# Kernel tuning notes

Measured on AMD Instinct MI355X. Metric: run time of the kernel, lower is better.

Reference implementation:

```python
import jax, jax.numpy as jnp
import numpy as np

B, T, IN_DIM, H = 128, 512, 128, 512


def _lstm_layer(x, W_ih, W_hh, b_ih, b_hh):
    """Single-layer batch-first LSTM (PyTorch gate order i,f,g,o).
    x: [B, T, D]. Returns (outputs [B, T, H], h_T [B, H], c_T [B, H])."""
    Bsz = x.shape[0]
    Hdim = W_hh.shape[1]
    # Precompute the input contribution for all timesteps: [T, B, 4H]
    xg = jnp.einsum('btd,gd->tbg', x, W_ih) + (b_ih + b_hh)

    def step(carry, xg_t):
        h, c = carry
        gates = xg_t + h @ W_hh.T  # [B, 4H]
        i, f, g, o = jnp.split(gates, 4, axis=-1)
        i = jax.nn.sigmoid(i)
        f = jax.nn.sigmoid(f)
        g = jnp.tanh(g)
        o = jax.nn.sigmoid(o)
        c = f * c + i * g
        h = o * jnp.tanh(c)
        return (h, c), h

    h0 = jnp.zeros((Bsz, Hdim), dtype=x.dtype)
    c0 = jnp.zeros((Bsz, Hdim), dtype=x.dtype)
    (hT, cT), outs = jax.lax.scan(step, (h0, c0), xg)
    return jnp.transpose(outs, (1, 0, 2)), hT, cT


def setup_inputs() -> dict:
    key = jax.random.key(0)
    ks = jax.random.split(key, 9)
    s1 = 1.0 / np.sqrt(H)
    inp = {
        'x': jax.random.normal(ks[0], (B, T, IN_DIM), dtype=jnp.float32),
        'W_ih1': jax.random.uniform(ks[1], (4 * H, IN_DIM), jnp.float32, -s1, s1),
        'W_hh1': jax.random.uniform(ks[2], (4 * H, H), jnp.float32, -s1, s1),
        'b_ih1': jax.random.uniform(ks[3], (4 * H,), jnp.float32, -s1, s1),
        'b_hh1': jax.random.uniform(ks[4], (4 * H,), jnp.float32, -s1, s1),
        'W_ih2': jax.random.uniform(ks[5], (4 * H, H), jnp.float32, -s1, s1),
        'W_hh2': jax.random.uniform(ks[6], (4 * H, H), jnp.float32, -s1, s1),
        'b_ih2': jax.random.uniform(ks[7], (4 * H,), jnp.float32, -s1, s1),
        'b_hh2': jax.random.uniform(ks[8], (4 * H,), jnp.float32, -s1, s1),
    }
    return inp


def reference(x, W_ih1, W_hh1, b_ih1, b_hh1, W_ih2, W_hh2, b_ih2, b_hh2):
    out1, _, _ = _lstm_layer(x, W_ih1, W_hh1, b_ih1, b_hh1)
    _, hT, cT = _lstm_layer(out1, W_ih2, W_hh2, b_ih2, b_hh2)
    # Match torch nn.LSTM final-state shape: [num_layers*dirs=1, B, H]
    return hT[None, :, :], cT[None, :, :]
```

## Files before the change

kernel.cpp:

```cpp
#include <hip/hip_runtime.h>
#include <stdint.h>
#include <stddef.h>


typedef __attribute__((ext_vector_type(8))) short short8;
typedef __attribute__((ext_vector_type(4))) float f32x4;
typedef unsigned long long u64;

#define DEV static __device__ __forceinline__
#define SCOPE_AGENT __HIP_MEMORY_SCOPE_AGENT

constexpr int TSEQ = 512;
constexpr int DIN  = 128;
constexpr int HDIM = 512;
constexpr int NCL  = 8;
constexpr int BB   = 16;
constexpr int NJ   = 32;
constexpr int COLS = 16;

DEV unsigned short f2bf(float f) {
  unsigned u = __float_as_uint(f);
  u += 0x7fffu + ((u >> 16) & 1u);
  return (unsigned short)(u >> 16);
}
DEV short8 pack8(float4 a, float4 b) {
  short8 r;
  r[0] = (short)f2bf(a.x); r[1] = (short)f2bf(a.y);
  r[2] = (short)f2bf(a.z); r[3] = (short)f2bf(a.w);
  r[4] = (short)f2bf(b.x); r[5] = (short)f2bf(b.y);
  r[6] = (short)f2bf(b.z); r[7] = (short)f2bf(b.w);
  return r;
}
DEV short8 mk8(u64 lo, u64 hi) {
  union { u64 q[2]; short8 v; } u;
  u.q[0] = lo; u.q[1] = hi; return u.v;
}
DEV f32x4 mfma16(short8 a, short8 b, f32x4 c) {
  return __builtin_amdgcn_mfma_f32_16x16x32_bf16(a, b, c, 0, 0, 0);
}
DEV float sigf(float v) { return 1.f / (1.f + __expf(-v)); }
DEV float tanh_(float v) {
  v = fminf(20.f, fmaxf(-20.f, v));
  float e = __expf(2.f * v);
  return (e - 1.f) / (e + 1.f);
}

__global__ void zero_ws(unsigned* p, int n) {
  int i = blockIdx.x * 256 + threadIdx.x;
  if (i < n)
    __hip_atomic_store(p + i, 0u, __ATOMIC_RELAXED, SCOPE_AGENT);
}

#define SWZ(row, idx) ((idx) ^ (((row) & 15) << 3))

__global__ __launch_bounds__(256, 1) void lstm_persist(
    const float* __restrict__ x,
    const float* __restrict__ Wih1, const float* __restrict__ Whh1,
    const float* __restrict__ bih1, const float* __restrict__ bhh1,
    const float* __restrict__ Wih2, const float* __restrict__ Whh2,
    const float* __restrict__ bih2, const float* __restrict__ bhh2,
    float* __restrict__ out,
    unsigned short* __restrict__ buf1,
    unsigned short* __restrict__ buf2,
    unsigned* __restrict__ flags)
{
  __shared__ short xs [16 * DIN];
  __shared__ short h1s[16 * HDIM];
  __shared__ short o1s[16 * HDIM];
  __shared__ short h2s[16 * HDIM];
  __shared__ float red1[4 * 16 * 66];
  __shared__ float red2[4 * 16 * 66];
  __shared__ float bias1s[64], bias2s[64];

  const int tid  = threadIdx.x;
  const int lane = tid & 63;
  const int lm   = lane & 15;
  const int lq   = lane >> 4;
  const int kq   = tid >> 6;

  const int bid     = blockIdx.x;
  const int cluster = bid & 7;
  const int j       = bid >> 3;
  const int cb      = cluster * BB;
  unsigned* flagA = flags + cluster * 64;
  unsigned* flagB = flags + cluster * 64 + NJ;

  short8 wf1[4][5];
  short8 wf2[4][8];
  #pragma unroll
  for (int g = 0; g < 4; ++g) {
    const int gr = g * HDIM + j * COLS + lm;
    #pragma unroll
    for (int sl = 0; sl < 5; ++sl) {
      const int k0 = (kq * 5 + sl) * 32 + 8 * lq;
      const float* src = (k0 < DIN) ? (Wih1 + (size_t)gr * DIN + k0)
                                    : (Whh1 + (size_t)gr * HDIM + (k0 - DIN));
      wf1[g][sl] = pack8(*(const float4*)src, *(const float4*)(src + 4));
    }
    #pragma unroll
    for (int sl = 0; sl < 8; ++sl) {
      const int k0 = (kq * 8 + sl) * 32 + 8 * lq;
      const float* src = (k0 < HDIM) ? (Wih2 + (size_t)gr * HDIM + k0)
                                     : (Whh2 + (size_t)gr * HDIM + (k0 - HDIM));
      wf2[g][sl] = pack8(*(const float4*)src, *(const float4*)(src + 4));
    }
  }
  if (tid < 64) {
    const int g = tid >> 4, nn = tid & 15;
    const int gr = g * HDIM + j * COLS + nn;
    bias1s[tid] = bih1[gr] + bhh1[gr];
    bias2s[tid] = bih2[gr] + bhh2[gr];
  }

  const int pm = tid >> 4, pnn = tid & 15;
  float c1 = 0.f, c2 = 0.f;

  for (int it = 0; it <= TSEQ + 2; ++it) {
    const bool l1 = (it < TSEQ);
    const bool l2 = (it >= 3);
    const int  t2 = it - 3;

    float4 xa, xb;
    if (l1) {
      const int row = tid >> 4, kc = tid & 15;
      const float* xp = x + ((size_t)(cb + row) * TSEQ + it) * DIN + kc * 8;
      xa = *(const float4*)xp; xb = *(const float4*)(xp + 4);
    }
    u64 o1t[8];
    if (l2) {
      const unsigned short* o1r =
          buf1 + (size_t)(((t2 & 3) * NCL + cluster) * BB) * HDIM;
      #pragma unroll
      for (int ci = 0; ci < 4; ++ci) {
        const int g = ci * 256 + tid, row = g >> 6, kc = g & 63;
        const u64* s = (const u64*)(o1r + (size_t)row * HDIM + kc * 8);
        o1t[2 * ci]     = __hip_atomic_load(s,     __ATOMIC_RELAXED, SCOPE_AGENT);
        o1t[2 * ci + 1] = __hip_atomic_load(s + 1, __ATOMIC_RELAXED, SCOPE_AGENT);
      }
    }

    if (it > 0) {
      if (kq == 0) {
        const unsigned tgtA = (unsigned)(l1 ? it : TSEQ);
        const unsigned tgtB = (it >= 4) ? (unsigned)(it - 1) : 0u;
        const unsigned tgt  = (lane < NJ) ? tgtA : tgtB;
        const unsigned* fl  = flagA + lane;
        while (true) {
          unsigned v = __hip_atomic_load(fl, __ATOMIC_RELAXED, SCOPE_AGENT);
          if (__all((int)(v >= tgt))) break;
          __builtin_amdgcn_s_sleep(1);
        }
      }
      __syncthreads();
    }

    if (l1) {
      const int row = tid >> 4, kc = tid & 15;
      *(short8*)(&xs[SWZ(row, row * DIN + kc * 8)]) = pack8(xa, xb);
    }
    if (l2) {
      #pragma unroll
      for (int ci = 0; ci < 4; ++ci) {
        const int g = ci * 256 + tid, row = g >> 6, kc = g & 63;
        *(short8*)(&o1s[SWZ(row, row * HDIM + kc * 8)]) =
            mk8(o1t[2 * ci], o1t[2 * ci + 1]);
      }
    }
    {
      u64 h1t[8], h2t[8];
      const unsigned short* h1r =
          buf1 + (size_t)((((it + 3) & 3) * NCL + cluster) * BB) * HDIM;
      const unsigned short* h2r =
          buf2 + (size_t)(((it & 1) * NCL + cluster) * BB) * HDIM;
      if (l1) {
        #pragma unroll
        for (int ci = 0; ci < 4; ++ci) {
          const int g = ci * 256 + tid, row = g >> 6, kc = g & 63;
          const u64* s = (const u64*)(h1r + (size_t)row * HDIM + kc * 8);
          h1t[2 * ci]     = __hip_atomic_load(s,     __ATOMIC_RELAXED, SCOPE_AGENT);
          h1t[2 * ci + 1] = __hip_atomic_load(s + 1, __ATOMIC_RELAXED, SCOPE_AGENT);
        }
      }
      if (l2) {
        #pragma unroll
        for (int ci = 0; ci < 4; ++ci) {
          const int g = ci * 256 + tid, row = g >> 6, kc = g & 63;
          const u64* s = (const u64*)(h2r + (size_t)row * HDIM + kc * 8);
          h2t[2 * ci]     = __hip_atomic_load(s,     __ATOMIC_RELAXED, SCOPE_AGENT);
          h2t[2 * ci + 1] = __hip_atomic_load(s + 1, __ATOMIC_RELAXED, SCOPE_AGENT);
        }
      }
      if (l1) {
        #pragma unroll
        for (int ci = 0; ci < 4; ++ci) {
          const int g = ci * 256 + tid, row = g >> 6, kc = g & 63;
          *(short8*)(&h1s[SWZ(row, row * HDIM + kc * 8)]) =
              mk8(h1t[2 * ci], h1t[2 * ci + 1]);
        }
      }
      if (l2) {
        #pragma unroll
        for (int ci = 0; ci < 4; ++ci) {
          const int g = ci * 256 + tid, row = g >> 6, kc = g & 63;
          *(short8*)(&h2s[SWZ(row, row * HDIM + kc * 8)]) =
              mk8(h2t[2 * ci], h2t[2 * ci + 1]);
        }
      }
    }
    __syncthreads();

    if (l1) {
      f32x4 z = {0.f, 0.f, 0.f, 0.f};
      f32x4 acc1[4] = {z, z, z, z};
      #pragma unroll
      for (int sl = 0; sl < 5; ++sl) {
        const int s = kq * 5 + sl;
        short8 a;
        if (s < 4)
          a = *(const short8*)(&xs[SWZ(lm, lm * DIN + s * 32 + 8 * lq)]);
        else
          a = *(const short8*)(&h1s[SWZ(lm, lm * HDIM + (s - 4) * 32 + 8 * lq)]);
        #pragma unroll
        for (int g = 0; g < 4; ++g) acc1[g] = mfma16(a, wf1[g][sl], acc1[g]);
      }
      #pragma unroll
      for (int g = 0; g < 4; ++g)
        #pragma unroll
        for (int r = 0; r < 4; ++r)
          red1[(kq * 16 + lq * 4 + r) * 66 + g * 16 + lm] = acc1[g][r];
    }
    __syncthreads();
    if (l1) {
      float p[4];
      #pragma unroll
      for (int g = 0; g < 4; ++g) {
        float v = bias1s[g * 16 + pnn];
        #pragma unroll
        for (int q = 0; q < 4; ++q) v += red1[(q * 16 + pm) * 66 + g * 16 + pnn];
        p[g] = v;
      }
      const float i_ = sigf(p[0]), f_ = sigf(p[1]);
      const float g_ = tanh_(p[2]), o_ = sigf(p[3]);
      c1 = f_ * c1 + i_ * g_;
      const float h1v = o_ * tanh_(c1);
      unsigned short* wp =
          buf1 + (size_t)(((it & 3) * NCL + cluster) * BB) * HDIM;
      __hip_atomic_store(&wp[pm * HDIM + j * COLS + pnn], f2bf(h1v),
                         __ATOMIC_RELAXED, SCOPE_AGENT);
    }
    __syncthreads();
    if (tid == 0 && l1)
      __hip_atomic_store(flagA + j, (unsigned)(it + 1),
                         __ATOMIC_RELAXED, SCOPE_AGENT);

    if (l2) {
      f32x4 z = {0.f, 0.f, 0.f, 0.f};
      f32x4 acc2[4] = {z, z, z, z};
      #pragma unroll
      for (int sl = 0; sl < 8; ++sl) {
        const int s2 = kq * 8 + sl;
        short8 a;
        if (s2 < 16)
          a = *(const short8*)(&o1s[SWZ(lm, lm * HDIM + s2 * 32 + 8 * lq)]);
        else
          a = *(const short8*)(&h2s[SWZ(lm, lm * HDIM + (s2 - 16) * 32 + 8 * lq)]);
        #pragma unroll
        for (int g = 0; g < 4; ++g) acc2[g] = mfma16(a, wf2[g][sl], acc2[g]);
      }
      #pragma unroll
      for (int g = 0; g < 4; ++g)
        #pragma unroll
        for (int r = 0; r < 4; ++r)
          red2[(kq * 16 + lq * 4 + r) * 66 + g * 16 + lm] = acc2[g][r];
    }
    __syncthreads();
    if (l2) {
      float p[4];
      #pragma unroll
      for (int g = 0; g < 4; ++g) {
        float v = bias2s[g * 16 + pnn];
        #pragma unroll
        for (int q = 0; q < 4; ++q) v += red2[(q * 16 + pm) * 66 + g * 16 + pnn];
        p[g] = v;
      }
      const float i_ = sigf(p[0]), f_ = sigf(p[1]);
      const float g_ = tanh_(p[2]), o_ = sigf(p[3]);
      c2 = f_ * c2 + i_ * g_;
      const float h2v = o_ * tanh_(c2);
      if (t2 < TSEQ - 1) {
        unsigned short* wp =
            buf2 + (size_t)((((it + 1) & 1) * NCL + cluster) * BB) * HDIM;
        __hip_atomic_store(&wp[pm * HDIM + j * COLS + pnn], f2bf(h2v),
                           __ATOMIC_RELAXED, SCOPE_AGENT);
      } else {
        const int b = cb + pm;
        out[(size_t)b * HDIM + j * COLS + pnn] = h2v;
        out[(size_t)128 * HDIM + (size_t)b * HDIM + j * COLS + pnn] = c2;
      }
    }
    __syncthreads();
    if (tid == 0 && l2)
      __hip_atomic_store(flagB + j, (unsigned)it,
                         __ATOMIC_RELAXED, SCOPE_AGENT);
  }
}

extern "C" void kernel_launch(void* const* d_in, const int* in_sizes, int n_in,
                              void* d_out, int out_size, void* d_ws, size_t ws_size,
                              hipStream_t stream) {
  const float* x    = (const float*)d_in[0];
  const float* Wih1 = (const float*)d_in[1];
  const float* Whh1 = (const float*)d_in[2];
  const float* bih1 = (const float*)d_in[3];
  const float* bhh1 = (const float*)d_in[4];
  const float* Wih2 = (const float*)d_in[5];
  const float* Whh2 = (const float*)d_in[6];
  const float* bih2 = (const float*)d_in[7];
  const float* bhh2 = (const float*)d_in[8];
  float* out = (float*)d_out;

  const size_t buf1Elems = (size_t)4 * NCL * BB * HDIM;
  const size_t buf2Elems = (size_t)2 * NCL * BB * HDIM;
  unsigned short* buf1 = (unsigned short*)d_ws;
  unsigned short* buf2 = buf1 + buf1Elems;
  unsigned* flags = (unsigned*)(buf2 + buf2Elems);

  const int nzero = (int)(((buf1Elems + buf2Elems) * 2 + NCL * 64 * 4) / 4);
  zero_ws<<<(nzero + 255) / 256, 256, 0, stream>>>((unsigned*)d_ws, nzero);
  lstm_persist<<<256, 256, 0, stream>>>(x, Wih1, Whh1, bih1, bhh1,
                                        Wih2, Whh2, bih2, bhh2,
                                        out, buf1, buf2, flags);
}
```

Before: 1.982 ms.

## Merge layer flags into one per-step barrier and batch hidden-state publishes

```diff
diff --git a/kernel.cpp b/kernel.cpp
--- a/kernel.cpp
+++ b/kernel.cpp
@@ -15,7 +15,6 @@
 constexpr int HDIM = 512;
 constexpr int NCL  = 8;
 constexpr int BB   = 16;
-constexpr int NJ   = 32;
 constexpr int COLS = 16;
 
 DEV unsigned short f2bf(float f) {
@@ -71,6 +70,7 @@
   __shared__ float red1[4 * 16 * 66];
   __shared__ float red2[4 * 16 * 66];
   __shared__ float bias1s[64], bias2s[64];
+  __shared__ unsigned short pub1s[256], pub2s[256];
 
   const int tid  = threadIdx.x;
   const int lane = tid & 63;
@@ -82,8 +82,7 @@
   const int cluster = bid & 7;
   const int j       = bid >> 3;
   const int cb      = cluster * BB;
-  unsigned* flagA = flags + cluster * 64;
-  unsigned* flagB = flags + cluster * 64 + NJ;
+  unsigned* flag = flags + cluster * 32;
 
   short8 wf1[4][5];
   short8 wf2[4][8];
@@ -141,10 +140,8 @@
 
     if (it > 0) {
       if (kq == 0) {
-        const unsigned tgtA = (unsigned)(l1 ? it : TSEQ);
-        const unsigned tgtB = (it >= 4) ? (unsigned)(it - 1) : 0u;
-        const unsigned tgt  = (lane < NJ) ? tgtA : tgtB;
-        const unsigned* fl  = flagA + lane;
+        const unsigned* fl = flag + (lane & 31);
+        const unsigned tgt = (unsigned)it;
         while (true) {
           unsigned v = __hip_atomic_load(fl, __ATOMIC_RELAXED, SCOPE_AGENT);
           if (__all((int)(v >= tgt))) break;
@@ -229,30 +226,6 @@
         for (int r = 0; r < 4; ++r)
           red1[(kq * 16 + lq * 4 + r) * 66 + g * 16 + lm] = acc1[g][r];
     }
-    __syncthreads();
-    if (l1) {
-      float p[4];
-      #pragma unroll
-      for (int g = 0; g < 4; ++g) {
-        float v = bias1s[g * 16 + pnn];
-        #pragma unroll
-        for (int q = 0; q < 4; ++q) v += red1[(q * 16 + pm) * 66 + g * 16 + pnn];
-        p[g] = v;
-      }
-      const float i_ = sigf(p[0]), f_ = sigf(p[1]);
-      const float g_ = tanh_(p[2]), o_ = sigf(p[3]);
-      c1 = f_ * c1 + i_ * g_;
-      const float h1v = o_ * tanh_(c1);
-      unsigned short* wp =
-          buf1 + (size_t)(((it & 3) * NCL + cluster) * BB) * HDIM;
-      __hip_atomic_store(&wp[pm * HDIM + j * COLS + pnn], f2bf(h1v),
-                         __ATOMIC_RELAXED, SCOPE_AGENT);
-    }
-    __syncthreads();
-    if (tid == 0 && l1)
-      __hip_atomic_store(flagA + j, (unsigned)(it + 1),
-                         __ATOMIC_RELAXED, SCOPE_AGENT);
-
     if (l2) {
       f32x4 z = {0.f, 0.f, 0.f, 0.f};
       f32x4 acc2[4] = {z, z, z, z};
@@ -274,6 +247,21 @@
           red2[(kq * 16 + lq * 4 + r) * 66 + g * 16 + lm] = acc2[g][r];
     }
     __syncthreads();
+
+    if (l1) {
+      float p[4];
+      #pragma unroll
+      for (int g = 0; g < 4; ++g) {
+        float v = bias1s[g * 16 + pnn];
+        #pragma unroll
+        for (int q = 0; q < 4; ++q) v += red1[(q * 16 + pm) * 66 + g * 16 + pnn];
+        p[g] = v;
+      }
+      const float i_ = sigf(p[0]), f_ = sigf(p[1]);
+      const float g_ = tanh_(p[2]), o_ = sigf(p[3]);
+      c1 = f_ * c1 + i_ * g_;
+      pub1s[pm * 16 + pnn] = f2bf(o_ * tanh_(c1));
+    }
     if (l2) {
       float p[4];
       #pragma unroll
@@ -288,10 +276,7 @@
       c2 = f_ * c2 + i_ * g_;
       const float h2v = o_ * tanh_(c2);
       if (t2 < TSEQ - 1) {
-        unsigned short* wp =
-            buf2 + (size_t)((((it + 1) & 1) * NCL + cluster) * BB) * HDIM;
-        __hip_atomic_store(&wp[pm * HDIM + j * COLS + pnn], f2bf(h2v),
-                           __ATOMIC_RELAXED, SCOPE_AGENT);
+        pub2s[pm * 16 + pnn] = f2bf(h2v);
       } else {
         const int b = cb + pm;
         out[(size_t)b * HDIM + j * COLS + pnn] = h2v;
@@ -299,9 +284,28 @@
       }
     }
     __syncthreads();
-    if (tid == 0 && l2)
-      __hip_atomic_store(flagB + j, (unsigned)it,
-                         __ATOMIC_RELAXED, SCOPE_AGENT);
+
+    if (kq == 0) {
+      const int row = lane >> 2, part = lane & 3;
+      if (l1) {
+        const u64 v = *(const u64*)&pub1s[row * 16 + part * 4];
+        unsigned short* wp =
+            buf1 + (size_t)(((it & 3) * NCL + cluster) * BB) * HDIM;
+        __hip_atomic_store((u64*)&wp[(size_t)row * HDIM + j * COLS + part * 4],
+                           v, __ATOMIC_RELAXED, SCOPE_AGENT);
+      }
+      if (l2 && t2 < TSEQ - 1) {
+        const u64 v = *(const u64*)&pub2s[row * 16 + part * 4];
+        unsigned short* wp =
+            buf2 + (size_t)(((t2 & 1) * NCL + cluster) * BB) * HDIM;
+        __hip_atomic_store((u64*)&wp[(size_t)row * HDIM + j * COLS + part * 4],
+                           v, __ATOMIC_RELAXED, SCOPE_AGENT);
+      }
+      asm volatile("s_waitcnt vmcnt(0)" ::: "memory");
+      if (lane == 0 && it <= TSEQ + 1)
+        __hip_atomic_store(flag + j, (unsigned)(it + 1),
+                           __ATOMIC_RELAXED, SCOPE_AGENT);
+    }
   }
 }
 
@@ -325,7 +329,7 @@
   unsigned short* buf2 = buf1 + buf1Elems;
   unsigned* flags = (unsigned*)(buf2 + buf2Elems);
 
-  const int nzero = (int)(((buf1Elems + buf2Elems) * 2 + NCL * 64 * 4) / 4);
+  const int nzero = (int)(((buf1Elems + buf2Elems) * 2 + NCL * 32 * 4) / 4);
   zero_ws<<<(nzero + 255) / 256, 256, 0, stream>>>((unsigned*)d_ws, nzero);
   lstm_persist<<<256, 256, 0, stream>>>(x, Wih1, Whh1, bih1, bhh1,
                                         Wih2, Whh2, bih2, bhh2,
```

Measured after the change: 2.349 ms. 1.19x slower.
